# Performance work log

Hardware: AMD Instinct MI355X
Metric: run time of the kernel (lower is better)

The kernel has to match this reference:

```python
import jax, jax.numpy as jnp
import numpy as np

TAU = 0.05
BIG_POSITIVE = 1.0e10
COS_EPS = 1e-8  # torch F.cosine_similarity default eps


def setup_inputs() -> dict:
    key = jax.random.key(0)
    k1, k2 = jax.random.split(key)
    b, d = 4096, 1024
    return {
        "batch_feat1": jax.random.normal(k1, (b, d), dtype=jnp.float32),
        "batch_feat2": jax.random.normal(k2, (b, d), dtype=jnp.float32),
        "input_mask": jnp.zeros((b,), dtype=jnp.int32),
    }


def reference(batch_feat1, batch_feat2, input_mask):
    # concat the two views: (2b, d)
    feat = jnp.concatenate([batch_feat1, batch_feat2], axis=0)
    bs = feat.shape[0]
    half = bs // 2

    # cosine similarity = normalize (clamped norm, as in torch) then GEMM
    norm = jnp.maximum(jnp.linalg.norm(feat, axis=-1, keepdims=True), COS_EPS)
    n = feat / norm
    similarity = n @ n.T  # (2b, 2b)

    # mask out self-similarity on the diagonal
    eye = jnp.eye(bs, dtype=similarity.dtype)
    logits = similarity / TAU - eye * BIG_POSITIVE

    idx = jnp.arange(half)
    y_true = jnp.concatenate([idx + half, idx])  # positive pair indices

    # weighted cross entropy: weight[c] = 1 - input_mask[c] (per-class weight)
    weight = (1 - jnp.concatenate([input_mask, input_mask], axis=0)).astype(logits.dtype)
    logp = jax.nn.log_softmax(logits, axis=-1)
    per_example = -jnp.take_along_axis(logp, y_true[:, None], axis=1)[:, 0]
    w = weight[y_true]
    loss = jnp.sum(w * per_example) / jnp.sum(w)
    return (loss, logits, y_true)
```

## Files before the change

### kernel.cpp

```cpp
#include <hip/hip_runtime.h>
#include <math.h>

#define BS 8192
#define HALF 4096
#define DIM 1024
#define TAU_INV 20.0f
#define BIGP 1.0e10f

typedef __attribute__((ext_vector_type(8))) short bf16x8;
typedef __attribute__((ext_vector_type(4))) float f32x4;

#define GLOAD_LDS16(g, l)                                              \
    __builtin_amdgcn_global_load_lds(                                  \
        (const __attribute__((address_space(1))) void*)(g),            \
        (__attribute__((address_space(3))) void*)(l), 16, 0, 0)

__device__ inline unsigned short f2bf(float f) {
    union { float f; unsigned int u; } c; c.f = f;
    unsigned int u = c.u;
    u += 0x7FFFu + ((u >> 16) & 1u);
    return (unsigned short)(u >> 16);
}

__global__ __launch_bounds__(256) void norm_kernel(const float* __restrict__ f1,
                                                   const float* __restrict__ f2,
                                                   unsigned short* __restrict__ nb) {
    const int row = blockIdx.x;
    const int t = threadIdx.x;
    const float* src = (row < HALF) ? (f1 + (size_t)row * DIM)
                                    : (f2 + (size_t)(row - HALF) * DIM);
    float4 v = reinterpret_cast<const float4*>(src)[t];
    float ss = v.x * v.x + v.y * v.y + v.z * v.z + v.w * v.w;
#pragma unroll
    for (int off = 32; off > 0; off >>= 1) ss += __shfl_down(ss, off, 64);
    __shared__ float red[4];
    if ((t & 63) == 0) red[t >> 6] = ss;
    __syncthreads();
    float tot = red[0] + red[1] + red[2] + red[3];
    float inv = 1.0f / fmaxf(sqrtf(tot), 1e-8f);
    ushort4 o;
    o.x = f2bf(v.x * inv);
    o.y = f2bf(v.y * inv);
    o.z = f2bf(v.z * inv);
    o.w = f2bf(v.w * inv);
    reinterpret_cast<ushort4*>(nb + (size_t)row * DIM)[t] = o;
}

#define BM 128
#define BN 128
#define BK 64

__global__ __launch_bounds__(256) void gemm_kernel(const unsigned short* __restrict__ nb,
                                                   float* __restrict__ logits,
                                                   float* __restrict__ psum,
                                                   float* __restrict__ targ) {
    __shared__ union {
        struct { unsigned short A[BM][BK]; unsigned short B[BN][BK]; } s;
        float T[64][129];
    } smem;
    __shared__ float rowpart[2][BM];
    __shared__ float colpart[2][BM];

    const int t = threadIdx.x;
    const int lane = t & 63;
    const int wid = t >> 6;
    const int wr = wid >> 1;
    const int wc = wid & 1;
    const int lo = lane & 15;
    const int hi = lane >> 4;

    const int id = blockIdx.x;
    int bx = (int)((sqrtf(8.0f * (float)id + 1.0f) - 1.0f) * 0.5f);
    while ((bx + 1) * (bx + 2) / 2 <= id) ++bx;
    while (bx * (bx + 1) / 2 > id) --bx;
    const int by = id - bx * (bx + 1) / 2;
    const bool diag = (bx == by);

    const int rowBase = by * BM;
    const int colBase = bx * BN;

    f32x4 acc[4][4];
#pragma unroll
    for (int m = 0; m < 4; ++m)
#pragma unroll
        for (int n = 0; n < 4; ++n) {
            acc[m][n][0] = 0.f; acc[m][n][1] = 0.f;
            acc[m][n][2] = 0.f; acc[m][n][3] = 0.f;
        }

    const int srow = lane >> 3;
    const int skoff = (((lane & 7) ^ srow) << 3);
    const char* Abase = (const char*)&smem.s.A[0][0];
    const char* Bbase = (const char*)&smem.s.B[0][0];
    const int rswz = (lo & 7) << 4;

    for (int kt = 0; kt < DIM; kt += BK) {
#pragma unroll
        for (int i = 0; i < 4; ++i) {
            const int chunk = wid * 4 + i;
            const int r = chunk * 8 + srow;
            const unsigned short* gA = nb + (size_t)(rowBase + r) * DIM + kt + skoff;
            GLOAD_LDS16(gA, (char*)&smem.s.A[0][0] + chunk * 1024);
            const unsigned short* gB = nb + (size_t)(colBase + r) * DIM + kt + skoff;
            GLOAD_LDS16(gB, (char*)&smem.s.B[0][0] + chunk * 1024);
        }
        __syncthreads();

#pragma unroll
        for (int ks = 0; ks < BK; ks += 32) {
            bf16x8 a[4], b[4];
#pragma unroll
            for (int m = 0; m < 4; ++m) {
                const int rr = wr * 64 + m * 16 + lo;
                a[m] = *reinterpret_cast<const bf16x8*>(
                    Abase + rr * 128 + ((ks * 2 + hi * 16) ^ rswz));
            }
#pragma unroll
            for (int n = 0; n < 4; ++n) {
                const int rr = wc * 64 + n * 16 + lo;
                b[n] = *reinterpret_cast<const bf16x8*>(
                    Bbase + rr * 128 + ((ks * 2 + hi * 16) ^ rswz));
            }
#pragma unroll
            for (int m = 0; m < 4; ++m)
#pragma unroll
                for (int n = 0; n < 4; ++n)
                    acc[m][n] = __builtin_amdgcn_mfma_f32_16x16x32_bf16(a[m], b[n], acc[m][n], 0, 0, 0);
        }
        __syncthreads();
    }

    float sums[16];
    float psn[4];
#pragma unroll
    for (int p = 0; p < 16; ++p) sums[p] = 0.f;
#pragma unroll
    for (int n = 0; n < 4; ++n) psn[n] = 0.f;

#pragma unroll
    for (int m = 0; m < 4; ++m) {
#pragma unroll
        for (int n = 0; n < 4; ++n) {
            const int col = colBase + wc * 64 + n * 16 + lo;
#pragma unroll
            for (int r = 0; r < 4; ++r) {
                const int row = rowBase + wr * 64 + m * 16 + hi * 4 + r;
                float v = acc[m][n][r] * TAU_INV;
                if (row == col) v -= BIGP;
                logits[(size_t)row * BS + col] = v;
                if (col == row + HALF) { targ[row] = v; targ[col] = v; }
                const float e = __expf(v - 20.0f);
                sums[m * 4 + r] += e;
                psn[n] += e;
            }
        }
    }

    float sel = 0.f;
#pragma unroll
    for (int p = 0; p < 16; ++p) {
        float s = sums[p];
        s += __shfl_xor(s, 1, 64);
        s += __shfl_xor(s, 2, 64);
        s += __shfl_xor(s, 4, 64);
        s += __shfl_xor(s, 8, 64);
        sel = (lo == p) ? s : sel;
    }
    rowpart[wc][wr * 64 + (lo >> 2) * 16 + hi * 4 + (lo & 3)] = sel;

    if (!diag) {
        float cs0 = psn[0], cs1 = psn[1], cs2 = psn[2], cs3 = psn[3];
        cs0 += __shfl_xor(cs0, 16, 64); cs0 += __shfl_xor(cs0, 32, 64);
        cs1 += __shfl_xor(cs1, 16, 64); cs1 += __shfl_xor(cs1, 32, 64);
        cs2 += __shfl_xor(cs2, 16, 64); cs2 += __shfl_xor(cs2, 32, 64);
        cs3 += __shfl_xor(cs3, 16, 64); cs3 += __shfl_xor(cs3, 32, 64);
        const float cw = (hi == 0) ? cs0 : (hi == 1) ? cs1 : (hi == 2) ? cs2 : cs3;
        colpart[wr][wc * 64 + hi * 16 + lo] = cw;
    }
    __syncthreads();

    if (t < BM) {
        psum[(size_t)bx * BS + rowBase + t] = rowpart[0][t] + rowpart[1][t];
        if (!diag)
            psum[(size_t)by * BS + colBase + t] = colpart[0][t] + colpart[1][t];
    }

    if (!diag) {
#pragma unroll
        for (int p = 0; p < 2; ++p) {
            __syncthreads();
            if (wc == p) {
#pragma unroll
                for (int m = 0; m < 4; ++m)
#pragma unroll
                    for (int n = 0; n < 4; ++n)
#pragma unroll
                        for (int r = 0; r < 4; ++r) {
                            const int ccol = n * 16 + lo;
                            const int crow = wr * 64 + m * 16 + hi * 4 + r;
                            smem.T[ccol][crow] = acc[m][n][r] * TAU_INV;
                        }
            }
            __syncthreads();
            const int tr = t >> 2;
            const int ch = t & 3;
            const float* Trow = &smem.T[tr][0];
            float* gdst = logits + (size_t)(colBase + p * 64 + tr) * BS + rowBase;
#pragma unroll
            for (int j = 0; j < 8; ++j) {
                f32x4 w = *reinterpret_cast<const f32x4*>(&Trow[ch * 4 + j * 16]);
                *reinterpret_cast<f32x4*>(&gdst[ch * 4 + j * 16]) = w;
            }
        }
    }
}

__global__ __launch_bounds__(256) void reduce_rows_kernel(const float* __restrict__ psum,
                                                          const float* __restrict__ targ,
                                                          const int* __restrict__ mask,
                                                          float* __restrict__ partials,
                                                          float* __restrict__ ytrue_out) {
    const int t = threadIdx.x;
    const int row = blockIdx.x * 256 + t;

    float total = 0.f;
#pragma unroll 8
    for (int cb = 0; cb < 64; ++cb) total += psum[(size_t)cb * BS + row];

    const float pe = -(targ[row] - 20.0f - logf(total));
    const float w = 1.0f - (float)mask[row & (HALF - 1)];
    ytrue_out[row] = (float)((row < HALF) ? row + HALF : row - HALF);

    float a = w * pe, b = w;
#pragma unroll
    for (int off = 32; off > 0; off >>= 1) {
        a += __shfl_down(a, off, 64);
        b += __shfl_down(b, off, 64);
    }
    __shared__ float ra[4], rb[4];
    if ((t & 63) == 0) { ra[t >> 6] = a; rb[t >> 6] = b; }
    __syncthreads();
    if (t == 0) {
        partials[blockIdx.x] = ra[0] + ra[1] + ra[2] + ra[3];
        partials[32 + blockIdx.x] = rb[0] + rb[1] + rb[2] + rb[3];
    }
}

__global__ void loss_kernel(const float* __restrict__ partials,
                            float* __restrict__ loss_out) {
    if (threadIdx.x == 0) {
        float A = 0.f, B = 0.f;
        for (int i = 0; i < 32; ++i) { A += partials[i]; B += partials[32 + i]; }
        loss_out[0] = A / B;
    }
}

extern "C" void kernel_launch(void* const* d_in, const int* in_sizes, int n_in,
                              void* d_out, int out_size, void* d_ws, size_t ws_size,
                              hipStream_t stream) {
    const float* f1 = (const float*)d_in[0];
    const float* f2 = (const float*)d_in[1];
    const int* mask = (const int*)d_in[2];
    float* out = (float*)d_out;

    unsigned short* nb = (unsigned short*)d_ws;
    float* psum = (float*)((char*)d_ws + (size_t)BS * DIM * 2);
    float* targ = psum + (size_t)64 * BS;
    float* partials = targ + BS;
    float* logits = out + 1;
    float* ytrue_out = out + 1 + (size_t)BS * BS;

    norm_kernel<<<BS, 256, 0, stream>>>(f1, f2, nb);

    const int ntri = (BS / BM) * (BS / BM + 1) / 2;
    gemm_kernel<<<ntri, 256, 0, stream>>>(nb, logits, psum, targ);

    reduce_rows_kernel<<<BS / 256, 256, 0, stream>>>(psum, targ, mask, partials, ytrue_out);
    loss_kernel<<<1, 64, 0, stream>>>(partials, out);
}
```

Measured before the change: 178.5 us.

## Fold temperature into normalization and write mirrored tile directly from registers

The 1/tau scale is folded into the normalized bf16 rows by multiplying each by sqrt(1/tau), so the GEMM accumulator already holds the logits and the per-element multiply disappears. The mirrored (transposed) tile is now stored straight from the MFMA accumulators as 16-byte vectors along the row direction, instead of being staged through an LDS transpose buffer with extra barriers. This removes the LDS round trip and the synchronisation, and shrinks shared memory, which may raise occupancy. The cost is less coalesced global stores, since each lane writes a separate 16-byte segment on a different output row. The bf16 values are also scaled before rounding, which slightly changes the numerics.

```diff
diff --git a/kernel.cpp b/kernel.cpp
--- a/kernel.cpp
+++ b/kernel.cpp
@@ -4,8 +4,8 @@
 #define BS 8192
 #define HALF 4096
 #define DIM 1024
-#define TAU_INV 20.0f
 #define BIGP 1.0e10f
+#define SQRT_TAU_INV 4.472135955f
 
 typedef __attribute__((ext_vector_type(8))) short bf16x8;
 typedef __attribute__((ext_vector_type(4))) float f32x4;
@@ -37,7 +37,7 @@
     if ((t & 63) == 0) red[t >> 6] = ss;
     __syncthreads();
     float tot = red[0] + red[1] + red[2] + red[3];
-    float inv = 1.0f / fmaxf(sqrtf(tot), 1e-8f);
+    float inv = SQRT_TAU_INV / fmaxf(sqrtf(tot), 1e-8f);
     ushort4 o;
     o.x = f2bf(v.x * inv);
     o.y = f2bf(v.y * inv);
@@ -54,10 +54,8 @@
                                                    float* __restrict__ logits,
                                                    float* __restrict__ psum,
                                                    float* __restrict__ targ) {
-    __shared__ union {
-        struct { unsigned short A[BM][BK]; unsigned short B[BN][BK]; } s;
-        float T[64][129];
-    } smem;
+    __shared__ unsigned short As[BM][BK];
+    __shared__ unsigned short Bs[BN][BK];
     __shared__ float rowpart[2][BM];
     __shared__ float colpart[2][BM];
 
@@ -90,8 +88,8 @@
 
     const int srow = lane >> 3;
     const int skoff = (((lane & 7) ^ srow) << 3);
-    const char* Abase = (const char*)&smem.s.A[0][0];
-    const char* Bbase = (const char*)&smem.s.B[0][0];
+    const char* Abase = (const char*)&As[0][0];
+    const char* Bbase = (const char*)&Bs[0][0];
     const int rswz = (lo & 7) << 4;
 
     for (int kt = 0; kt < DIM; kt += BK) {
@@ -100,9 +98,9 @@
             const int chunk = wid * 4 + i;
             const int r = chunk * 8 + srow;
             const unsigned short* gA = nb + (size_t)(rowBase + r) * DIM + kt + skoff;
-            GLOAD_LDS16(gA, (char*)&smem.s.A[0][0] + chunk * 1024);
+            GLOAD_LDS16(gA, (char*)&As[0][0] + chunk * 1024);
             const unsigned short* gB = nb + (size_t)(colBase + r) * DIM + kt + skoff;
-            GLOAD_LDS16(gB, (char*)&smem.s.B[0][0] + chunk * 1024);
+            GLOAD_LDS16(gB, (char*)&Bs[0][0] + chunk * 1024);
         }
         __syncthreads();
 
@@ -145,13 +143,25 @@
 #pragma unroll
             for (int r = 0; r < 4; ++r) {
                 const int row = rowBase + wr * 64 + m * 16 + hi * 4 + r;
-                float v = acc[m][n][r] * TAU_INV;
+                float v = acc[m][n][r];
                 if (row == col) v -= BIGP;
                 logits[(size_t)row * BS + col] = v;
                 if (col == row + HALF) { targ[row] = v; targ[col] = v; }
                 const float e = __expf(v - 20.0f);
                 sums[m * 4 + r] += e;
                 psn[n] += e;
+            }
+        }
+    }
+
+    if (!diag) {
+#pragma unroll
+        for (int m = 0; m < 4; ++m) {
+            const int trow0 = rowBase + wr * 64 + m * 16 + hi * 4;
+#pragma unroll
+            for (int n = 0; n < 4; ++n) {
+                const int col = colBase + wc * 64 + n * 16 + lo;
+                *reinterpret_cast<f32x4*>(&logits[(size_t)col * BS + trow0]) = acc[m][n];
             }
         }
     }
@@ -184,35 +194,6 @@
         if (!diag)
             psum[(size_t)by * BS + colBase + t] = colpart[0][t] + colpart[1][t];
     }
-
-    if (!diag) {
-#pragma unroll
-        for (int p = 0; p < 2; ++p) {
-            __syncthreads();
-            if (wc == p) {
-#pragma unroll
-                for (int m = 0; m < 4; ++m)
-#pragma unroll
-                    for (int n = 0; n < 4; ++n)
-#pragma unroll
-                        for (int r = 0; r < 4; ++r) {
-                            const int ccol = n * 16 + lo;
-                            const int crow = wr * 64 + m * 16 + hi * 4 + r;
-                            smem.T[ccol][crow] = acc[m][n][r] * TAU_INV;
-                        }
-            }
-            __syncthreads();
-            const int tr = t >> 2;
-            const int ch = t & 3;
-            const float* Trow = &smem.T[tr][0];
-            float* gdst = logits + (size_t)(colBase + p * 64 + tr) * BS + rowBase;
-#pragma unroll
-            for (int j = 0; j < 8; ++j) {
-                f32x4 w = *reinterpret_cast<const f32x4*>(&Trow[ch * 4 + j * 16]);
-                *reinterpret_cast<f32x4*>(&gdst[ch * 4 + j * 16]) = w;
-            }
-        }
-    }
 }
 
 __global__ __launch_bounds__(256) void reduce_rows_kernel(const float* __restrict__ psum,
```

After: 170.9 us. 1.04x faster.
